# Performance work log

Hardware: AMD Instinct MI355X
Metric: run time of the kernel (lower is better)

## Reference

```python
import jax, jax.numpy as jnp
import numpy as np

CONF_THRESH = 0.5   # foreground objectness threshold (module default)
NMS_THRESH = 0.4    # IoU suppression threshold (module default)
SCORE_THRESH = 0.3  # hard-coded max-class-score filter in forward

BS, NUM_BOXES, NUM_ATTRS = 2, 6300, 85  # 80 classes


def setup_inputs() -> dict:
    key = jax.random.key(0)
    # uniform [0,1): boxes live in the unit square and overlap heavily,
    # objectness/class scores frequently exceed the thresholds.
    x = jax.random.uniform(key, (BS, NUM_BOXES, NUM_ATTRS), dtype=jnp.float32)
    return {"x": x}


def _nms_keep(corners, scores, cls_idx, valid):
    """Per-image, per-class greedy NMS.

    corners: [N,4] (x1,y1,x2,y2), scores: [N] objectness, cls_idx: [N] int,
    valid: [N] bool. Returns keep mask [N] bool. Faithful to the torch loop:
    sort by objectness desc, greedily keep the top box of each class and
    suppress same-class boxes with IoU >= nms_thresh (torch keeps iou < t).
    """
    n = scores.shape[0]
    order = jnp.argsort(-scores)      # descending by objectness (column 4)
    rank = jnp.argsort(order)         # rank[j] = position of box j in order

    x1, y1, x2, y2 = corners[:, 0], corners[:, 1], corners[:, 2], corners[:, 3]
    area = (x2 - x1) * (y2 - y1)
    iw = jnp.maximum(jnp.minimum(x2[:, None], x2[None, :]) -
                     jnp.maximum(x1[:, None], x1[None, :]), 0.0)
    ih = jnp.maximum(jnp.minimum(y2[:, None], y2[None, :]) -
                     jnp.maximum(y1[:, None], y1[None, :]), 0.0)
    inter = iw * ih                                   # [N,N]
    iou = inter / (area[:, None] + area[None, :] - inter + 1e-16)
    same_cls = cls_idx[:, None] == cls_idx[None, :]    # [N,N]

    def body(r, keep):
        i = order[r]
        # suppress strictly lower-ranked, still-alive, same-class overlaps
        sup = (iou[i] >= NMS_THRESH) & same_cls[i] & (rank > r)
        return jnp.where(keep[i], keep & ~sup, keep)

    return jax.lax.fori_loop(0, n, body, valid)


def reference(x):
    """x: [bs, N, 5+num_classes]. Returns detections [bs, N, 8]:
    [batch_idx, x1, y1, x2, y2, p_obj, max_cls_score, cls_idx],
    zeroed for suppressed / filtered boxes (fixed-shape analogue of the
    variable-length torch output)."""
    conf_mask = x[..., 4] > CONF_THRESH
    xm = x * conf_mask[..., None].astype(x.dtype)

    # center -> corner transform
    xy, wh = xm[..., :2], xm[..., 2:4]
    corners = jnp.concatenate([xy - wh * 0.5, xy + wh * 0.5], axis=-1)  # [bs,N,4]

    p_obj = xm[..., 4]
    cls_scores = xm[..., 5:]
    max_score = jnp.max(cls_scores, axis=-1)
    cls_idx = jnp.argmax(cls_scores, axis=-1)
    valid = conf_mask & (max_score > SCORE_THRESH)

    keep = jax.vmap(_nms_keep)(corners, p_obj, cls_idx, valid)  # [bs,N] bool

    bs, n = p_obj.shape
    batch_idx = jnp.broadcast_to(
        jnp.arange(bs, dtype=x.dtype)[:, None], (bs, n))
    det = jnp.concatenate([
        batch_idx[..., None], corners, p_obj[..., None],
        max_score[..., None], cls_idx.astype(x.dtype)[..., None]], axis=-1)
    return det * keep[..., None].astype(x.dtype)
```

## Files before the change

### kernel.cpp

```cpp
#include <hip/hip_runtime.h>

#define BSZ   2
#define NBOX  6300
#define NATTR 85
#define NCLS  80
#define CAP   256

typedef unsigned long long ull;

static __device__ __forceinline__ ull mask_for(int rem) {
  if (rem <= 0) return 0ull;
  if (rem >= 64) return ~0ull;
  return (1ull << rem) - 1ull;
}

__global__ __launch_bounds__(256) void prep_kernel(
    const float* __restrict__ x,
    int* __restrict__ vcls,
    float* __restrict__ out) {
  int gid  = blockIdx.x * blockDim.x + threadIdx.x;
  int box  = gid >> 6;
  int lane = threadIdx.x & 63;

  const float* p = x + (long)box * NATTR;
  float r0 = p[lane];
  float r1 = (lane < NATTR - 64) ? p[64 + lane] : -1.0f;

  float c0 = (lane >= 5) ? r0 : -1.0f;
  float v; int vi;
  if (r1 > c0) { v = r1; vi = 64 + lane; }
  else         { v = c0; vi = lane; }

  for (int off = 32; off > 0; off >>= 1) {
    float ov = __shfl_xor(v, off);
    int   oi = __shfl_xor(vi, off);
    if (ov > v || (ov == v && oi < vi)) { v = ov; vi = oi; }
  }

  float cx  = __shfl(r0, 0), cy = __shfl(r0, 1);
  float w   = __shfl(r0, 2), h  = __shfl(r0, 3);
  float obj = __shfl(r0, 4);
  bool valid = (obj > 0.5f) && (v > 0.3f);
  int  img   = box >= NBOX ? 1 : 0;
  int  cls   = vi - 5;

  if (lane == 0) {
    vcls[box] = valid ? cls : -1;
    float4 a, b;
    if (valid) {
      float hw = w * 0.5f, hh = h * 0.5f;
      a = make_float4((float)img, cx - hw, cy - hh, cx + hw);
      b = make_float4(cy + hh, obj, v, (float)cls);
    } else {
      a = make_float4(0.f, 0.f, 0.f, 0.f);
      b = a;
    }
    float4* o = (float4*)(out + (long)box * 8);
    o[0] = a; o[1] = b;
  }
}

__global__ __launch_bounds__(256) void nms_kernel(
    const int* __restrict__ vcls,
    float* out) {
  __shared__ int   wlist[4][CAP];
  __shared__ int   wcnt[4];
  __shared__ int   sbi[CAP];
  __shared__ float ssc[CAP];
  __shared__ float px1[CAP], py1[CAP], px2[CAP], py2[CAP];
  __shared__ int   pbi[CAP];

  int bc   = blockIdx.x;
  int img  = bc / NCLS;
  int cls  = bc - img * NCLS;
  int t    = threadIdx.x;
  int lane = t & 63;
  int w    = t >> 6;
  const int* v = vcls + img * NBOX;

  int base = w * 1600;
  int vals[25];
#pragma unroll
  for (int i = 0; i < 25; i++) {
    int idx = base + i * 64 + lane;
    vals[i] = (idx < NBOX) ? v[idx] : -1;
  }
  int cnt = 0;
#pragma unroll
  for (int i = 0; i < 25; i++) {
    bool match = (vals[i] == cls);
    ull  m = __ballot(match);
    if (match) {
      int pos = cnt + __popcll(m & ((1ull << lane) - 1ull));
      if (pos < CAP) wlist[w][pos] = base + i * 64 + lane;
    }
    cnt += __popcll(m);
  }
  if (lane == 0) wcnt[w] = cnt < CAP ? cnt : CAP;
  __syncthreads();

  int off = 0, total = 0;
  for (int j = 0; j < 4; j++) {
    int c = wcnt[j];
    if (j < w) off += c;
    total += c;
  }
  int k = total < CAP ? total : CAP;
  if (k == 0) return;

  for (int j = lane; j < wcnt[w]; j += 64) {
    int d = off + j;
    if (d < CAP) sbi[d] = wlist[w][j];
  }
  __syncthreads();

  if (k <= 64) {
    if (w == 0) {
      int j = lane;
      float x1 = 0.f, y1 = 0.f, x2 = 0.f, y2 = 0.f, sc = 0.f;
      int bi = 0;
      if (j < k) {
        bi = sbi[j];
        const float4* o = (const float4*)(out + ((long)img * NBOX + bi) * 8);
        float4 a = o[0], b = o[1];
        x1 = a.y; y1 = a.z; x2 = a.w; y2 = b.x; sc = b.y;
      }
      int rank = 0;
      for (int i = 0; i < k; i++) {
        float si  = __shfl(sc, i);
        int   bii = __shfl(bi, i);
        rank += (si > sc) || (si == sc && bii < bi);
      }
      if (j >= k) rank = j;

      int r4 = rank << 2;
      x1 = __int_as_float(__builtin_amdgcn_ds_permute(r4, __float_as_int(x1)));
      y1 = __int_as_float(__builtin_amdgcn_ds_permute(r4, __float_as_int(y1)));
      x2 = __int_as_float(__builtin_amdgcn_ds_permute(r4, __float_as_int(x2)));
      y2 = __int_as_float(__builtin_amdgcn_ds_permute(r4, __float_as_int(y2)));
      bi = __builtin_amdgcn_ds_permute(r4, bi);

      float ar = (x2 - x1) * (y2 - y1);

      ull keep = mask_for(k);
      for (int r = 0; r < k - 1; r++) {
        if (!((keep >> r) & 1ull)) continue;
        float X1 = __shfl(x1, r), Y1 = __shfl(y1, r);
        float X2 = __shfl(x2, r), Y2 = __shfl(y2, r);
        float AR = __shfl(ar, r);
        float iw = fminf(X2, x2) - fmaxf(X1, x1);
        float ih = fminf(Y2, y2) - fmaxf(Y1, y1);
        iw = fmaxf(iw, 0.0f); ih = fmaxf(ih, 0.0f);
        float inter = iw * ih;
        float iou = inter / (AR + ar - inter + 1e-16f);
        keep &= ~__ballot(iou >= 0.4f && lane > r);
      }

      if (lane < k && !((keep >> lane) & 1ull)) {
        float4 z = make_float4(0.f, 0.f, 0.f, 0.f);
        float4* o = (float4*)(out + ((long)img * NBOX + bi) * 8);
        o[0] = z; o[1] = z;
      }
    }
    return;
  }

  float bx1 = 0, by1 = 0, bx2 = 0, by2 = 0, bobj = 0;
  int   bidx = 0;
  if (t < k) {
    bidx = sbi[t];
    const float4* o = (const float4*)(out + ((long)img * NBOX + bidx) * 8);
    float4 a = o[0], b = o[1];
    bx1 = a.y; by1 = a.z; bx2 = a.w; by2 = b.x; bobj = b.y;
    ssc[t] = bobj;
  }
  __syncthreads();

  if (t < k) {
    int rank = 0;
    for (int j = 0; j < k; j++) {
      float sj = ssc[j];
      rank += (sj > bobj) || (sj == bobj && sbi[j] < bidx);
    }
    px1[rank] = bx1; py1[rank] = by1;
    px2[rank] = bx2; py2[rank] = by2;
    pbi[rank] = bidx;
  }
  __syncthreads();

  if (w == 0) {
    float mx1[4], my1[4], mx2[4], my2[4], mar[4];
    int   mbi[4];
#pragma unroll
    for (int s = 0; s < 4; s++) {
      int e = s * 64 + lane;
      if (e < k) {
        mx1[s] = px1[e]; my1[s] = py1[e];
        mx2[s] = px2[e]; my2[s] = py2[e];
        mbi[s] = pbi[e];
        mar[s] = (mx2[s] - mx1[s]) * (my2[s] - my1[s]);
      } else {
        mx1[s] = 0; my1[s] = 0; mx2[s] = 0; my2[s] = 0; mar[s] = 0; mbi[s] = 0;
      }
    }
    ull km0 = mask_for(k);
    ull km1 = mask_for(k - 64);
    ull km2 = mask_for(k - 128);
    ull km3 = mask_for(k - 192);

    for (int r = 0; r < k - 1; r++) {
      ull cur = (r < 64) ? km0 : (r < 128) ? km1 : (r < 192) ? km2 : km3;
      if (!((cur >> (r & 63)) & 1ull)) continue;
      float X1 = px1[r], Y1 = py1[r], X2 = px2[r], Y2 = py2[r];
      float ar = (X2 - X1) * (Y2 - Y1);
      {
        int e = lane;
        float iw = fminf(X2, mx2[0]) - fmaxf(X1, mx1[0]);
        float ih = fminf(Y2, my2[0]) - fmaxf(Y1, my1[0]);
        iw = fmaxf(iw, 0.0f); ih = fmaxf(ih, 0.0f);
        float inter = iw * ih;
        float iou = inter / (ar + mar[0] - inter + 1e-16f);
        km0 &= ~__ballot(iou >= 0.4f && e > r && e < k);
      }
      if (k > 64) {
        int e = 64 + lane;
        float iw = fminf(X2, mx2[1]) - fmaxf(X1, mx1[1]);
        float ih = fminf(Y2, my2[1]) - fmaxf(Y1, my1[1]);
        iw = fmaxf(iw, 0.0f); ih = fmaxf(ih, 0.0f);
        float inter = iw * ih;
        float iou = inter / (ar + mar[1] - inter + 1e-16f);
        km1 &= ~__ballot(iou >= 0.4f && e > r && e < k);
      }
      if (k > 128) {
        int e = 128 + lane;
        float iw = fminf(X2, mx2[2]) - fmaxf(X1, mx1[2]);
        float ih = fminf(Y2, my2[2]) - fmaxf(Y1, my1[2]);
        iw = fmaxf(iw, 0.0f); ih = fmaxf(ih, 0.0f);
        float inter = iw * ih;
        float iou = inter / (ar + mar[2] - inter + 1e-16f);
        km2 &= ~__ballot(iou >= 0.4f && e > r && e < k);
      }
      if (k > 192) {
        int e = 192 + lane;
        float iw = fminf(X2, mx2[3]) - fmaxf(X1, mx1[3]);
        float ih = fminf(Y2, my2[3]) - fmaxf(Y1, my1[3]);
        iw = fmaxf(iw, 0.0f); ih = fmaxf(ih, 0.0f);
        float inter = iw * ih;
        float iou = inter / (ar + mar[3] - inter + 1e-16f);
        km3 &= ~__ballot(iou >= 0.4f && e > r && e < k);
      }
    }

    float4 z = make_float4(0.f, 0.f, 0.f, 0.f);
#pragma unroll
    for (int s = 0; s < 4; s++) {
      ull kms = (s == 0) ? km0 : (s == 1) ? km1 : (s == 2) ? km2 : km3;
      int e = s * 64 + lane;
      if (e < k && !((kms >> lane) & 1ull)) {
        float4* o = (float4*)(out + ((long)img * NBOX + mbi[s]) * 8);
        o[0] = z; o[1] = z;
      }
    }
  }
}

extern "C" void kernel_launch(void* const* d_in, const int* in_sizes, int n_in,
                              void* d_out, int out_size, void* d_ws, size_t ws_size,
                              hipStream_t stream) {
  const float* x = (const float*)d_in[0];
  float* out = (float*)d_out;
  int* vcls = (int*)d_ws;

  prep_kernel<<<(BSZ * NBOX * 64) / 256, 256, 0, stream>>>(x, vcls, out);
  nms_kernel<<<BSZ * NCLS, 256, 0, stream>>>(vcls, out);
}
```

Before: 69.68 us.

## Fuse prep and NMS kernels into one persistent kernel with a flag barrier

Merges the per-box decode kernel and the per-class NMS kernel into one 512-block launch. Each wave decodes boxes in a grid-stride loop, then publishes a magic value to a per-block flag. The 160 NMS blocks spin on all flags before starting. This removes the second kernel launch and its inter-kernel gap, but it relies on all 512 blocks being resident at once. The flags are never reset, so on later calls the barrier may pass before the current decode has finished.

Result: slower. 103.8 us (+48.9%).

```diff
diff --git a/kernel.cpp b/kernel.cpp
--- a/kernel.cpp
+++ b/kernel.cpp
@@ -5,6 +5,8 @@
 #define NATTR 85
 #define NCLS  80
 #define CAP   256
+#define GRID  512
+#define MAGIC 0x3C6E1A2Bu
 
 typedef unsigned long long ull;
 
@@ -14,54 +16,10 @@
   return (1ull << rem) - 1ull;
 }
 
-__global__ __launch_bounds__(256) void prep_kernel(
+__global__ __launch_bounds__(256) void fused_kernel(
     const float* __restrict__ x,
     int* __restrict__ vcls,
-    float* __restrict__ out) {
-  int gid  = blockIdx.x * blockDim.x + threadIdx.x;
-  int box  = gid >> 6;
-  int lane = threadIdx.x & 63;
-
-  const float* p = x + (long)box * NATTR;
-  float r0 = p[lane];
-  float r1 = (lane < NATTR - 64) ? p[64 + lane] : -1.0f;
-
-  float c0 = (lane >= 5) ? r0 : -1.0f;
-  float v; int vi;
-  if (r1 > c0) { v = r1; vi = 64 + lane; }
-  else         { v = c0; vi = lane; }
-
-  for (int off = 32; off > 0; off >>= 1) {
-    float ov = __shfl_xor(v, off);
-    int   oi = __shfl_xor(vi, off);
-    if (ov > v || (ov == v && oi < vi)) { v = ov; vi = oi; }
-  }
-
-  float cx  = __shfl(r0, 0), cy = __shfl(r0, 1);
-  float w   = __shfl(r0, 2), h  = __shfl(r0, 3);
-  float obj = __shfl(r0, 4);
-  bool valid = (obj > 0.5f) && (v > 0.3f);
-  int  img   = box >= NBOX ? 1 : 0;
-  int  cls   = vi - 5;
-
-  if (lane == 0) {
-    vcls[box] = valid ? cls : -1;
-    float4 a, b;
-    if (valid) {
-      float hw = w * 0.5f, hh = h * 0.5f;
-      a = make_float4((float)img, cx - hw, cy - hh, cx + hw);
-      b = make_float4(cy + hh, obj, v, (float)cls);
-    } else {
-      a = make_float4(0.f, 0.f, 0.f, 0.f);
-      b = a;
-    }
-    float4* o = (float4*)(out + (long)box * 8);
-    o[0] = a; o[1] = b;
-  }
-}
-
-__global__ __launch_bounds__(256) void nms_kernel(
-    const int* __restrict__ vcls,
+    unsigned int* __restrict__ flags,
     float* out) {
   __shared__ int   wlist[4][CAP];
   __shared__ int   wcnt[4];
@@ -70,12 +28,72 @@
   __shared__ float px1[CAP], py1[CAP], px2[CAP], py2[CAP];
   __shared__ int   pbi[CAP];
 
-  int bc   = blockIdx.x;
-  int img  = bc / NCLS;
-  int cls  = bc - img * NCLS;
   int t    = threadIdx.x;
   int lane = t & 63;
   int w    = t >> 6;
+
+  int gw = blockIdx.x * 4 + w;
+  for (int box = gw; box < BSZ * NBOX; box += GRID * 4) {
+    const float* p = x + (long)box * NATTR;
+    float r0 = p[lane];
+    float r1 = (lane < NATTR - 64) ? p[64 + lane] : -1.0f;
+
+    float c0 = (lane >= 5) ? r0 : -1.0f;
+    float v; int vi;
+    if (r1 > c0) { v = r1; vi = 64 + lane; }
+    else         { v = c0; vi = lane; }
+
+    for (int off = 32; off > 0; off >>= 1) {
+      float ov = __shfl_xor(v, off);
+      int   oi = __shfl_xor(vi, off);
+      if (ov > v || (ov == v && oi < vi)) { v = ov; vi = oi; }
+    }
+
+    float cx  = __shfl(r0, 0), cy = __shfl(r0, 1);
+    float bw  = __shfl(r0, 2), bh = __shfl(r0, 3);
+    float obj = __shfl(r0, 4);
+    bool valid = (obj > 0.5f) && (v > 0.3f);
+    int  img   = box >= NBOX ? 1 : 0;
+    int  cls   = vi - 5;
+
+    if (lane == 0) {
+      vcls[box] = valid ? cls : -1;
+      float4 a, b;
+      if (valid) {
+        float hw = bw * 0.5f, hh = bh * 0.5f;
+        a = make_float4((float)img, cx - hw, cy - hh, cx + hw);
+        b = make_float4(cy + hh, obj, v, (float)cls);
+      } else {
+        a = make_float4(0.f, 0.f, 0.f, 0.f);
+        b = a;
+      }
+      float4* o = (float4*)(out + (long)box * 8);
+      o[0] = a; o[1] = b;
+    }
+  }
+
+  __syncthreads();
+  if (t == 0) {
+    __threadfence();
+    __hip_atomic_store(&flags[blockIdx.x], MAGIC,
+                       __ATOMIC_RELEASE, __HIP_MEMORY_SCOPE_AGENT);
+  }
+  if (blockIdx.x >= BSZ * NCLS) return;
+
+  {
+    bool ok;
+    do {
+      unsigned a = __hip_atomic_load(&flags[t],       __ATOMIC_ACQUIRE,
+                                     __HIP_MEMORY_SCOPE_AGENT);
+      unsigned b = __hip_atomic_load(&flags[t + 256], __ATOMIC_ACQUIRE,
+                                     __HIP_MEMORY_SCOPE_AGENT);
+      ok = (a == MAGIC) && (b == MAGIC);
+    } while (!__syncthreads_and(ok));
+  }
+
+  int bc  = blockIdx.x;
+  int img = bc / NCLS;
+  int cls = bc - img * NCLS;
   const int* v = vcls + img * NBOX;
 
   int base = w * 1600;
@@ -270,7 +288,7 @@
   const float* x = (const float*)d_in[0];
   float* out = (float*)d_out;
   int* vcls = (int*)d_ws;
-
-  prep_kernel<<<(BSZ * NBOX * 64) / 256, 256, 0, stream>>>(x, vcls, out);
-  nms_kernel<<<BSZ * NCLS, 256, 0, stream>>>(vcls, out);
+  unsigned int* flags = (unsigned int*)(vcls + BSZ * NBOX);
+
+  fused_kernel<<<GRID, 256, 0, stream>>>(x, vcls, flags, out);
 }
```
